# Kernel optimization log

Hardware: AMD Instinct MI355X
Metric: run time of the kernel (lower is better)

Reference implementation:

```python
import jax, jax.numpy as jnp
import numpy as np

NUM_USERS = 100_000
NUM_ITEMS = 50_000
N_TOTAL = 150_100
EMBED_DIM = 64
NUM_LAYERS = 3
N_EDGES = 3_000_000
BATCH = 4096


def setup_inputs() -> dict:
    key = jax.random.key(0)
    k1, k2, k3, k4, k5, k6 = jax.random.split(key, 6)
    node_emb = jax.random.normal(k1, (N_TOTAL, EMBED_DIM), dtype=jnp.float32) * 0.1
    # COO sparse normalized adjacency (static irregular pattern)
    adj_row = jax.random.randint(k2, (N_EDGES,), 0, N_TOTAL, dtype=jnp.int32)
    adj_col = jax.random.randint(k3, (N_EDGES,), 0, N_TOTAL, dtype=jnp.int32)
    adj_val = jax.random.uniform(k4, (N_EDGES,), dtype=jnp.float32) * 0.05
    user_ids = jax.random.randint(k5, (BATCH,), 0, NUM_USERS, dtype=jnp.int32)
    item_ids = jax.random.randint(k6, (BATCH,), 0, NUM_ITEMS, dtype=jnp.int32)
    return {"node_emb": node_emb, "adj_val": adj_val, "adj_row": adj_row,
            "adj_col": adj_col, "user_ids": user_ids, "item_ids": item_ids}


def reference(node_emb, adj_val, adj_row, adj_col, user_ids, item_ids):
    # LightGCN propagation: K sparse SpMM layers, running mean over K+1 embeddings
    emb = node_emb                       # [N, D] layer-0
    acc = emb                            # running sum instead of stack+mean
    for _ in range(NUM_LAYERS):
        # SpMM: out[r] += val * emb[c]   (COO scatter-add)
        msgs = adj_val[:, None] * emb[adj_col]          # [E, D]
        emb = jax.ops.segment_sum(msgs, adj_row, num_segments=N_TOTAL)
        acc = acc + emb
    final = acc / jnp.float32(NUM_LAYERS + 1)           # mean over layers
    users = final[:NUM_USERS]
    items = final[NUM_USERS:NUM_USERS + NUM_ITEMS]
    u = users[user_ids]                                 # [B, D]
    i = items[item_ids]                                 # [B, D]
    return (u * i).sum(axis=-1)                         # [B]
```

## Files before the change

### kernel.cpp

```cpp
#include <hip/hip_runtime.h>

#define N_TOTAL    150100
#define NUM_USERS  100000
#define DIM        64
#define BSHIFT     8
#define BROWS      (1 << BSHIFT)
#define NBUK       ((N_TOTAL + BROWS - 1) / BROWS)
#define EPB        4096
#define EPT        16
#define CAP        5632
#define RSP        260

#define VSCALE     262144.0f
#define VINV       (1.0f / 262144.0f)

__device__ __forceinline__ int wave_incl_scan(int x, int lane) {
    #pragma unroll
    for (int off = 1; off < 64; off <<= 1) {
        int y = __shfl_up(x, off, 64);
        if (lane >= off) x += y;
    }
    return x;
}

__device__ __forceinline__ float ub0(unsigned w) { return (float)(w & 0xFFu); }
__device__ __forceinline__ float ub1(unsigned w) { return (float)((w >> 8) & 0xFFu); }
__device__ __forceinline__ float ub2(unsigned w) { return (float)((w >> 16) & 0xFFu); }
__device__ __forceinline__ float ub3(unsigned w) { return (float)(w >> 24); }

__device__ __forceinline__ unsigned quant_pack(float4 f, float inv) {
    int a = __float2int_rn(f.x * inv) + 128;
    int b = __float2int_rn(f.y * inv) + 128;
    int c = __float2int_rn(f.z * inv) + 128;
    int d = __float2int_rn(f.w * inv) + 128;
    a = min(max(a, 0), 255); b = min(max(b, 0), 255);
    c = min(max(c, 0), 255); d = min(max(d, 0), 255);
    return (unsigned)a | ((unsigned)b << 8) | ((unsigned)c << 16) | ((unsigned)d << 24);
}

__global__ void convert_quant(const float4* __restrict__ in4,
                              unsigned* __restrict__ q, float* __restrict__ sc,
                              int* __restrict__ gcount) {
    int t = blockIdx.x * blockDim.x + threadIdx.x;
    if (t < NBUK) gcount[t] = 0;
    int r = t >> 4, sl = t & 15;
    if (r >= N_TOTAL) return;
    float4 f = in4[(size_t)r * 16 + sl];
    float m = fmaxf(fmaxf(fabsf(f.x), fabsf(f.y)), fmaxf(fabsf(f.z), fabsf(f.w)));
    #pragma unroll
    for (int off = 1; off < 16; off <<= 1) m = fmaxf(m, __shfl_xor(m, off, 64));
    float inv = (m > 1e-30f) ? 127.0f / m : 0.0f;
    q[(size_t)r * 16 + sl] = quant_pack(f, inv);
    if (sl == 0) sc[r] = m * (1.0f / 127.0f);
}

__global__ void __launch_bounds__(256, 4) fill_buckets(
        const int* __restrict__ rows, const int* __restrict__ cols,
        const float* __restrict__ vals, int n_edges,
        int* __restrict__ gcount,
        uint2* __restrict__ epk8) {
    __shared__ unsigned      payb[EPB];
    __shared__ unsigned char rowb[EPB];
    __shared__ short         tgtb[EPB];
    __shared__ int hist[NBUK];
    __shared__ int pref[NBUK];
    __shared__ int cur[NBUK];
    __shared__ int loc[NBUK];
    __shared__ int wtot[4];
    const int tid = threadIdx.x;
    const int lane = tid & 63, wid = tid >> 6;
    const int base = blockIdx.x * EPB;
    int end = base + EPB; if (end > n_edges) end = n_edges;
    const int cnt = end - base;

    for (int i = tid; i < NBUK; i += 256) hist[i] = 0;

    unsigned pay[EPT];
    unsigned er[EPT];
    __syncthreads();

    if (cnt == EPB) {
        #pragma unroll
        for (int g = 0; g < 4; ++g) {
            const int e = base + (g * 256 + tid) * 4;
            int4   r4 = *(const int4*)(rows + e);
            int4   c4 = *(const int4*)(cols + e);
            float4 v4 = *(const float4*)(vals + e);
            int rr[4] = { r4.x, r4.y, r4.z, r4.w };
            int cc[4] = { c4.x, c4.y, c4.z, c4.w };
            float vv[4] = { v4.x, v4.y, v4.z, v4.w };
            #pragma unroll
            for (int k = 0; k < 4; ++k) {
                const int j = g * 4 + k;
                int q = (int)(vv[k] * VSCALE + 0.5f);
                if (q > 16383) q = 16383;
                pay[j] = ((unsigned)cc[k] << 14) | (unsigned)q;
                er[j]  = (unsigned)rr[k];
                atomicAdd(&hist[rr[k] >> BSHIFT], 1);
            }
        }
    } else {
        #pragma unroll
        for (int g = 0; g < 4; ++g) {
            const int e0 = base + (g * 256 + tid) * 4;
            #pragma unroll
            for (int k = 0; k < 4; ++k) {
                const int j = g * 4 + k;
                const int e = e0 + k;
                if (e < end) {
                    int r = rows[e];
                    int q = (int)(vals[e] * VSCALE + 0.5f);
                    if (q > 16383) q = 16383;
                    pay[j] = ((unsigned)cols[e] << 14) | (unsigned)q;
                    er[j]  = (unsigned)r;
                    atomicAdd(&hist[r >> BSHIFT], 1);
                } else {
                    er[j] = 0xFFFFFFFFu;
                }
            }
        }
    }
    __syncthreads();

    for (int b = tid; b < NBUK; b += 256) {
        int h = hist[b];
        loc[b] = h ? atomicAdd(&gcount[b], h) : 0;
    }
    const int t0 = tid * 3;
    int t1 = t0 + 3; if (t1 > NBUK) t1 = NBUK;
    int s = 0;
    for (int i = t0; i < t1; ++i) s += hist[i];
    int incl = wave_incl_scan(s, lane);
    if (lane == 63) wtot[wid] = incl;
    __syncthreads();
    int wofs = 0;
    for (int w = 0; w < wid; ++w) wofs += wtot[w];
    int run = incl + wofs - s;
    for (int i = t0; i < t1; ++i) {
        int h = hist[i];
        pref[i] = run;
        cur[i] = run;
        run += h;
    }
    __syncthreads();

    #pragma unroll
    for (int j = 0; j < EPT; ++j) {
        unsigned r = er[j];
        if (r != 0xFFFFFFFFu) {
            int b = (int)(r >> BSHIFT);
            int pos = atomicAdd(&cur[b], 1);
            payb[pos] = pay[j];
            rowb[pos] = (unsigned char)(r & (BROWS - 1));
            tgtb[pos] = (short)b;
        }
    }
    __syncthreads();

    for (int i = tid; i < cnt; i += 256) {
        int b = tgtb[i];
        int o = loc[b] + (i - pref[b]);
        if (o < CAP) {
            epk8[(size_t)b * CAP + o] = make_uint2(payb[i], (unsigned)rowb[i]);
        }
    }
}

__global__ void __launch_bounds__(256) bucket_sort(
        uint2* __restrict__ epk8,
        const int* __restrict__ gcount,
        int* __restrict__ rs) {
    __shared__ unsigned      buf[CAP];
    __shared__ unsigned char rbuf[CAP];
    __shared__ int hist[BROWS];
    __shared__ int curl[BROWS];
    __shared__ int wtot[4];
    const int tid = threadIdx.x;
    const int lane = tid & 63, wid = tid >> 6;
    const int b = blockIdx.x;
    const size_t k0 = (size_t)b * CAP;
    int cnt = gcount[b]; if (cnt > CAP) cnt = CAP;

    hist[tid] = 0;
    __syncthreads();
    for (int i = tid; i < cnt; i += 256) {
        uint2 e = epk8[k0 + i];
        buf[i]  = e.x;
        rbuf[i] = (unsigned char)e.y;
        atomicAdd(&hist[e.y & 255u], 1);
    }
    __syncthreads();
    int s = hist[tid];
    int incl = wave_incl_scan(s, lane);
    if (lane == 63) wtot[wid] = incl;
    __syncthreads();
    int wofs = 0;
    for (int w = 0; w < wid; ++w) wofs += wtot[w];
    int ex = incl + wofs - s;
    const int rbase = b << BSHIFT;
    int nrow = N_TOTAL - rbase; if (nrow > BROWS) nrow = BROWS;
    const int o0 = 2 * b * CAP;
    if (tid < nrow) rs[b * RSP + tid] = o0 + ex;
    if (tid == 0) rs[b * RSP + nrow] = o0 + cnt;
    curl[tid] = ex;
    __syncthreads();
    unsigned* out = (unsigned*)epk8;
    for (int i = tid; i < cnt; i += 256) {
        int rl = rbuf[i];
        int pos = atomicAdd(&curl[rl], 1);
        out[o0 + pos] = buf[i];
    }
}


__global__ void spmm_q8(const unsigned* __restrict__ qt,
                        const float* __restrict__ sc,
                        const int* __restrict__ rs,
                        const unsigned* __restrict__ epk,
                        unsigned* __restrict__ qo,
                        float* __restrict__ so) {
    int t = blockIdx.x * blockDim.x + threadIdx.x;
    int r = t >> 4;
    int sl = t & 15;
    int lane = threadIdx.x & 63;
    int subbase = lane & 48;
    if (r >= N_TOTAL) return;
    const int* rsb = rs + (r >> BSHIFT) * RSP + (r & (BROWS - 1));
    int k0 = rsb[0], k1 = rsb[1];
    float4 s = make_float4(0.f, 0.f, 0.f, 0.f);
    float corr = 0.f;
    for (int kb = k0; kb < k1; kb += 16) {
        int cnt = k1 - kb; if (cnt > 16) cnt = 16;
        unsigned pr = (sl < cnt) ? epk[kb + sl] : 0u;
        int j = 0;
        for (; j + 4 <= cnt; j += 4) {
            unsigned e0 = (unsigned)__shfl((int)pr, subbase + j + 0, 64);
            unsigned e1 = (unsigned)__shfl((int)pr, subbase + j + 1, 64);
            unsigned e2 = (unsigned)__shfl((int)pr, subbase + j + 2, 64);
            unsigned e3 = (unsigned)__shfl((int)pr, subbase + j + 3, 64);
            int c0 = e0 >> 14, c1 = e1 >> 14, c2 = e2 >> 14, c3 = e3 >> 14;
            unsigned w0 = qt[(size_t)c0 * 16 + sl];
            unsigned w1 = qt[(size_t)c1 * 16 + sl];
            unsigned w2 = qt[(size_t)c2 * 16 + sl];
            unsigned w3 = qt[(size_t)c3 * 16 + sl];
            float vs0 = (float)(e0 & 16383u) * VINV * sc[c0];
            float vs1 = (float)(e1 & 16383u) * VINV * sc[c1];
            float vs2 = (float)(e2 & 16383u) * VINV * sc[c2];
            float vs3 = (float)(e3 & 16383u) * VINV * sc[c3];
            corr += vs0 + vs1 + vs2 + vs3;
            s.x += vs0 * ub0(w0); s.y += vs0 * ub1(w0);
            s.z += vs0 * ub2(w0); s.w += vs0 * ub3(w0);
            s.x += vs1 * ub0(w1); s.y += vs1 * ub1(w1);
            s.z += vs1 * ub2(w1); s.w += vs1 * ub3(w1);
            s.x += vs2 * ub0(w2); s.y += vs2 * ub1(w2);
            s.z += vs2 * ub2(w2); s.w += vs2 * ub3(w2);
            s.x += vs3 * ub0(w3); s.y += vs3 * ub1(w3);
            s.z += vs3 * ub2(w3); s.w += vs3 * ub3(w3);
        }
        for (; j < cnt; ++j) {
            unsigned e = (unsigned)__shfl((int)pr, subbase + j, 64);
            int c = e >> 14;
            unsigned w = qt[(size_t)c * 16 + sl];
            float vs = (float)(e & 16383u) * VINV * sc[c];
            corr += vs;
            s.x += vs * ub0(w); s.y += vs * ub1(w);
            s.z += vs * ub2(w); s.w += vs * ub3(w);
        }
    }
    float c128 = 128.0f * corr;
    s.x -= c128; s.y -= c128; s.z -= c128; s.w -= c128;
    float m = fmaxf(fmaxf(fabsf(s.x), fabsf(s.y)), fmaxf(fabsf(s.z), fabsf(s.w)));
    #pragma unroll
    for (int off = 1; off < 16; off <<= 1) m = fmaxf(m, __shfl_xor(m, off, 64));
    float inv = (m > 1e-30f) ? 127.0f / m : 0.0f;
    qo[(size_t)r * 16 + sl] = quant_pack(s, inv);
    if (sl == 0) so[r] = m * (1.0f / 127.0f);
}

__device__ __forceinline__ float4 dec4(unsigned w, float s) {
    return make_float4(s * (ub0(w) - 128.0f), s * (ub1(w) - 128.0f),
                       s * (ub2(w) - 128.0f), s * (ub3(w) - 128.0f));
}

__device__ __forceinline__ float4 rowsum_q8(const unsigned* __restrict__ qt,
                                            const float* __restrict__ sc,
                                            const int* __restrict__ rs,
                                            const unsigned* __restrict__ epk,
                                            int r, int sl, int subbase) {
    const int* rsb = rs + (r >> BSHIFT) * RSP + (r & (BROWS - 1));
    int k0 = rsb[0], k1 = rsb[1];
    float4 s = make_float4(0.f, 0.f, 0.f, 0.f);
    float corr = 0.f;
    for (int kb = k0; kb < k1; kb += 16) {
        int cnt = k1 - kb; if (cnt > 16) cnt = 16;
        unsigned pr = (sl < cnt) ? epk[kb + sl] : 0u;
        for (int j = 0; j < cnt; ++j) {
            unsigned e = (unsigned)__shfl((int)pr, subbase + j, 64);
            int c = e >> 14;
            unsigned w = qt[(size_t)c * 16 + sl];
            float vs = (float)(e & 16383u) * VINV * sc[c];
            corr += vs;
            s.x += vs * ub0(w); s.y += vs * ub1(w);
            s.z += vs * ub2(w); s.w += vs * ub3(w);
        }
    }
    float c128 = 128.0f * corr;
    s.x -= c128; s.y -= c128; s.z -= c128; s.w -= c128;
    return s;
}

__global__ void final_dot_fused(const float4* __restrict__ emb4,
                                const unsigned* __restrict__ q1,
                                const float* __restrict__ s1,
                                const unsigned* __restrict__ q2,
                                const float* __restrict__ s2,
                                const int* __restrict__ rs,
                                const unsigned* __restrict__ epk,
                                const int* __restrict__ user_ids,
                                const int* __restrict__ item_ids,
                                float* __restrict__ out, int batch) {
    int t = blockIdx.x * blockDim.x + threadIdx.x;
    int b = t >> 4, sl = t & 15;
    int lane = threadIdx.x & 63;
    int subbase = lane & 48;
    if (b >= batch) return;
    int u = user_ids[b];
    int iN = NUM_USERS + item_ids[b];

    float4 lu = rowsum_q8(q2, s2, rs, epk, u, sl, subbase);
    float4 li = rowsum_q8(q2, s2, rs, epk, iN, sl, subbase);

    float4 nu = emb4[(size_t)u * 16 + sl];
    float4 au = dec4(q1[(size_t)u * 16 + sl], s1[u]);
    float4 bu = dec4(q2[(size_t)u * 16 + sl], s2[u]);
    float4 ni = emb4[(size_t)iN * 16 + sl];
    float4 ai = dec4(q1[(size_t)iN * 16 + sl], s1[iN]);
    float4 bi = dec4(q2[(size_t)iN * 16 + sl], s2[iN]);

    float ux = nu.x + au.x + bu.x + lu.x;
    float uy = nu.y + au.y + bu.y + lu.y;
    float uz = nu.z + au.z + bu.z + lu.z;
    float uw = nu.w + au.w + bu.w + lu.w;
    float ix = ni.x + ai.x + bi.x + li.x;
    float iy = ni.y + ai.y + bi.y + li.y;
    float iz = ni.z + ai.z + bi.z + li.z;
    float iw = ni.w + ai.w + bi.w + li.w;

    float s = ux * ix + uy * iy + uz * iz + uw * iw;
    #pragma unroll
    for (int off = 8; off > 0; off >>= 1) s += __shfl_down(s, off, 64);
    if (sl == 0) out[b] = s * (1.0f / 16.0f);
}


static inline size_t align256(size_t x) { return (x + 255) & ~(size_t)255; }

extern "C" void kernel_launch(void* const* d_in, const int* in_sizes, int n_in,
                              void* d_out, int out_size, void* d_ws, size_t ws_size,
                              hipStream_t stream) {
    const float* node_emb = (const float*)d_in[0];
    const float* adj_val  = (const float*)d_in[1];
    const int*   adj_row  = (const int*)d_in[2];
    const int*   adj_col  = (const int*)d_in[3];
    const int*   user_ids = (const int*)d_in[4];
    const int*   item_ids = (const int*)d_in[5];
    float* out = (float*)d_out;

    const int n_edges = in_sizes[1];
    const int batch   = in_sizes[4];

    const size_t qtab_bytes = (size_t)N_TOTAL * 16 * sizeof(unsigned);
    const size_t sc_bytes   = (size_t)N_TOTAL * sizeof(float);

    char* p = (char*)d_ws;
    size_t off = 0;
    unsigned* q0 = (unsigned*)(p + off); off = align256(off + qtab_bytes);
    unsigned* q1 = (unsigned*)(p + off); off = align256(off + qtab_bytes);
    unsigned* q2 = (unsigned*)(p + off); off = align256(off + qtab_bytes);
    float* s0    = (float*)(p + off);    off = align256(off + sc_bytes);
    float* s1    = (float*)(p + off);    off = align256(off + sc_bytes);
    float* s2    = (float*)(p + off);    off = align256(off + sc_bytes);
    int* gcount  = (int*)(p + off);      off = align256(off + (size_t)NBUK * sizeof(int));
    int* rs      = (int*)(p + off);      off = align256(off + (size_t)NBUK * RSP * sizeof(int));
    uint2* epk8  = (uint2*)(p + off);    off = align256(off + (size_t)NBUK * CAP * sizeof(uint2));
    (void)ws_size;

    const int nbf = (n_edges + EPB - 1) / EPB;
    const int rblocks = ((N_TOTAL * 16) + 255) / 256;

    convert_quant<<<rblocks, 256, 0, stream>>>(
        (const float4*)node_emb, q0, s0, gcount);

    fill_buckets<<<nbf, 256, 0, stream>>>(adj_row, adj_col, adj_val, n_edges,
                                          gcount, epk8);
    bucket_sort<<<NBUK, 256, 0, stream>>>(epk8, gcount, rs);

    const unsigned* epk = (const unsigned*)epk8;

    spmm_q8<<<rblocks, 256, 0, stream>>>(q0, s0, rs, epk, q1, s1);
    spmm_q8<<<rblocks, 256, 0, stream>>>(q1, s1, rs, epk, q2, s2);

    {
        int threads = batch * 16;
        final_dot_fused<<<(threads + 255) / 256, 256, 0, stream>>>(
            (const float4*)node_emb, q1, s1, q2, s2, rs, epk,
            user_ids, item_ids, out, batch);
    }
}
```

Baseline: 279.8 us.

## Process each SpMM row with 4 threads using 16-byte quantized loads

Changes the SpMM kernel from 16 threads per row, each loading 4 bytes, to 4 threads per row, each loading 16 bytes (uint4) of the int8 embedding row. Edges are fetched 4 at a time, broadcast by shuffle, and accumulated into four float4 registers. The output is written as a single uint4 store. This cuts the thread count and the per-edge shuffle and index overhead, and issues wider gathers. In exchange each thread does 4x the work, uses more registers, and has less parallelism to hide gather latency.

```diff
diff --git a/kernel.cpp b/kernel.cpp
--- a/kernel.cpp
+++ b/kernel.cpp
@@ -213,6 +213,23 @@
 }
 
 
+#define SPMM_EDGE(J)                                                          \
+    {                                                                         \
+        unsigned e = (unsigned)__shfl((int)pr, subbase + (J), 64);            \
+        int c = (int)(e >> 14);                                               \
+        uint4 w = *(const uint4*)(qt + (size_t)c * 16 + (sl << 2));           \
+        float vs = (float)(e & 16383u) * VINV * sc[c];                        \
+        corr += vs;                                                           \
+        sA.x += vs * ub0(w.x); sA.y += vs * ub1(w.x);                         \
+        sA.z += vs * ub2(w.x); sA.w += vs * ub3(w.x);                         \
+        sB.x += vs * ub0(w.y); sB.y += vs * ub1(w.y);                         \
+        sB.z += vs * ub2(w.y); sB.w += vs * ub3(w.y);                         \
+        sC.x += vs * ub0(w.z); sC.y += vs * ub1(w.z);                         \
+        sC.z += vs * ub2(w.z); sC.w += vs * ub3(w.z);                         \
+        sD.x += vs * ub0(w.w); sD.y += vs * ub1(w.w);                         \
+        sD.z += vs * ub2(w.w); sD.w += vs * ub3(w.w);                         \
+    }
+
 __global__ void spmm_q8(const unsigned* __restrict__ qt,
                         const float* __restrict__ sc,
                         const int* __restrict__ rs,
@@ -220,60 +237,43 @@
                         unsigned* __restrict__ qo,
                         float* __restrict__ so) {
     int t = blockIdx.x * blockDim.x + threadIdx.x;
-    int r = t >> 4;
-    int sl = t & 15;
+    int r = t >> 2;
+    int sl = t & 3;
     int lane = threadIdx.x & 63;
-    int subbase = lane & 48;
+    int subbase = lane & 60;
     if (r >= N_TOTAL) return;
     const int* rsb = rs + (r >> BSHIFT) * RSP + (r & (BROWS - 1));
     int k0 = rsb[0], k1 = rsb[1];
-    float4 s = make_float4(0.f, 0.f, 0.f, 0.f);
+    float4 sA = make_float4(0.f, 0.f, 0.f, 0.f);
+    float4 sB = make_float4(0.f, 0.f, 0.f, 0.f);
+    float4 sC = make_float4(0.f, 0.f, 0.f, 0.f);
+    float4 sD = make_float4(0.f, 0.f, 0.f, 0.f);
     float corr = 0.f;
-    for (int kb = k0; kb < k1; kb += 16) {
-        int cnt = k1 - kb; if (cnt > 16) cnt = 16;
+    for (int kb = k0; kb < k1; kb += 4) {
+        int cnt = k1 - kb; if (cnt > 4) cnt = 4;
         unsigned pr = (sl < cnt) ? epk[kb + sl] : 0u;
-        int j = 0;
-        for (; j + 4 <= cnt; j += 4) {
-            unsigned e0 = (unsigned)__shfl((int)pr, subbase + j + 0, 64);
-            unsigned e1 = (unsigned)__shfl((int)pr, subbase + j + 1, 64);
-            unsigned e2 = (unsigned)__shfl((int)pr, subbase + j + 2, 64);
-            unsigned e3 = (unsigned)__shfl((int)pr, subbase + j + 3, 64);
-            int c0 = e0 >> 14, c1 = e1 >> 14, c2 = e2 >> 14, c3 = e3 >> 14;
-            unsigned w0 = qt[(size_t)c0 * 16 + sl];
-            unsigned w1 = qt[(size_t)c1 * 16 + sl];
-            unsigned w2 = qt[(size_t)c2 * 16 + sl];
-            unsigned w3 = qt[(size_t)c3 * 16 + sl];
-            float vs0 = (float)(e0 & 16383u) * VINV * sc[c0];
-            float vs1 = (float)(e1 & 16383u) * VINV * sc[c1];
-            float vs2 = (float)(e2 & 16383u) * VINV * sc[c2];
-            float vs3 = (float)(e3 & 16383u) * VINV * sc[c3];
-            corr += vs0 + vs1 + vs2 + vs3;
-            s.x += vs0 * ub0(w0); s.y += vs0 * ub1(w0);
-            s.z += vs0 * ub2(w0); s.w += vs0 * ub3(w0);
-            s.x += vs1 * ub0(w1); s.y += vs1 * ub1(w1);
-            s.z += vs1 * ub2(w1); s.w += vs1 * ub3(w1);
-            s.x += vs2 * ub0(w2); s.y += vs2 * ub1(w2);
-            s.z += vs2 * ub2(w2); s.w += vs2 * ub3(w2);
-            s.x += vs3 * ub0(w3); s.y += vs3 * ub1(w3);
-            s.z += vs3 * ub2(w3); s.w += vs3 * ub3(w3);
-        }
-        for (; j < cnt; ++j) {
-            unsigned e = (unsigned)__shfl((int)pr, subbase + j, 64);
-            int c = e >> 14;
-            unsigned w = qt[(size_t)c * 16 + sl];
-            float vs = (float)(e & 16383u) * VINV * sc[c];
-            corr += vs;
-            s.x += vs * ub0(w); s.y += vs * ub1(w);
-            s.z += vs * ub2(w); s.w += vs * ub3(w);
+        if (cnt == 4) {
+            SPMM_EDGE(0) SPMM_EDGE(1) SPMM_EDGE(2) SPMM_EDGE(3)
+        } else {
+            for (int j = 0; j < cnt; ++j) SPMM_EDGE(j)
         }
     }
     float c128 = 128.0f * corr;
-    s.x -= c128; s.y -= c128; s.z -= c128; s.w -= c128;
-    float m = fmaxf(fmaxf(fabsf(s.x), fabsf(s.y)), fmaxf(fabsf(s.z), fabsf(s.w)));
-    #pragma unroll
-    for (int off = 1; off < 16; off <<= 1) m = fmaxf(m, __shfl_xor(m, off, 64));
+    sA.x -= c128; sA.y -= c128; sA.z -= c128; sA.w -= c128;
+    sB.x -= c128; sB.y -= c128; sB.z -= c128; sB.w -= c128;
+    sC.x -= c128; sC.y -= c128; sC.z -= c128; sC.w -= c128;
+    sD.x -= c128; sD.y -= c128; sD.z -= c128; sD.w -= c128;
+    float mA = fmaxf(fmaxf(fabsf(sA.x), fabsf(sA.y)), fmaxf(fabsf(sA.z), fabsf(sA.w)));
+    float mB = fmaxf(fmaxf(fabsf(sB.x), fabsf(sB.y)), fmaxf(fabsf(sB.z), fabsf(sB.w)));
+    float mC = fmaxf(fmaxf(fabsf(sC.x), fabsf(sC.y)), fmaxf(fabsf(sC.z), fabsf(sC.w)));
+    float mD = fmaxf(fmaxf(fabsf(sD.x), fabsf(sD.y)), fmaxf(fabsf(sD.z), fabsf(sD.w)));
+    float m = fmaxf(fmaxf(mA, mB), fmaxf(mC, mD));
+    m = fmaxf(m, __shfl_xor(m, 1, 64));
+    m = fmaxf(m, __shfl_xor(m, 2, 64));
     float inv = (m > 1e-30f) ? 127.0f / m : 0.0f;
-    qo[(size_t)r * 16 + sl] = quant_pack(s, inv);
+    uint4 o = make_uint4(quant_pack(sA, inv), quant_pack(sB, inv),
+                         quant_pack(sC, inv), quant_pack(sD, inv));
+    *(uint4*)(qo + (size_t)r * 16 + (sl << 2)) = o;
     if (sl == 0) so[r] = m * (1.0f / 127.0f);
 }
 
@@ -387,6 +387,7 @@
 
     const int nbf = (n_edges + EPB - 1) / EPB;
     const int rblocks = ((N_TOTAL * 16) + 255) / 256;
+    const int sblocks = ((N_TOTAL * 4) + 255) / 256;
 
     convert_quant<<<rblocks, 256, 0, stream>>>(
         (const float4*)node_emb, q0, s0, gcount);
@@ -397,8 +398,8 @@
 
     const unsigned* epk = (const unsigned*)epk8;
 
-    spmm_q8<<<rblocks, 256, 0, stream>>>(q0, s0, rs, epk, q1, s1);
-    spmm_q8<<<rblocks, 256, 0, stream>>>(q1, s1, rs, epk, q2, s2);
+    spmm_q8<<<sblocks, 256, 0, stream>>>(q0, s0, rs, epk, q1, s1);
+    spmm_q8<<<sblocks, 256, 0, stream>>>(q1, s1, rs, epk, q2, s2);
 
     {
         int threads = batch * 16;
```

After: 300.3 us. 1.07x slower.
